# Kernel optimization log

Measured on AMD Instinct MI355X. Metric: run time of the kernel, lower is better.

## Reference

```python
import jax, jax.numpy as jnp
import numpy as np

BAG = 15          # bag_size
STEPS = 5
LAM = 1e-3        # anti_hebb_lambda
PS = 8            # patch_size
IM = 28           # image_size
DEN = IM - PS     # position normalization denominator (=20)
KEEP = 0.1        # 1 - recurrent_sparsity


def _ln(h, gamma, beta, eps=1e-5):
    mu = jnp.mean(h, axis=-1, keepdims=True)
    var = jnp.mean((h - mu) ** 2, axis=-1, keepdims=True)
    return (h - mu) * jax.lax.rsqrt(var + eps) * gamma + beta


def _patch(img, pos):
    # img: [IM, IM], pos: [2] int32 -> flattened PSxPS patch [PS*PS]
    return jax.lax.dynamic_slice(img, (pos[0], pos[1]), (PS, PS)).reshape(PS * PS)

_extract = jax.vmap(_patch)  # [B,IM,IM], [B,2] -> [B, PS*PS]


def setup_inputs() -> dict:
    key = jax.random.key(0)
    ks = jax.random.split(key, 8)
    B = 65536
    x = jax.random.normal(ks[0], (B, 1, IM, IM), jnp.float32)
    in_dim = PS * PS + 2
    Wi = jax.random.normal(ks[1], (BAG, in_dim), jnp.float32) * np.sqrt(2.0 / in_dim)
    bi = jnp.zeros((BAG,), jnp.float32)
    gamma = jnp.ones((BAG,), jnp.float32)
    beta = jnp.zeros((BAG,), jnp.float32)
    mask = (jax.random.uniform(ks[2], (BAG, BAG)) < KEEP).astype(jnp.float32)
    R = jax.random.normal(ks[3], (BAG, BAG), jnp.float32) * np.sqrt(2.0 / BAG) * mask
    rb = jnp.zeros((BAG,), jnp.float32)
    Wc = jax.random.normal(ks[4], (2, BAG), jnp.float32) * np.sqrt(2.0 / BAG)
    bc = jnp.zeros((2,), jnp.float32)
    Wo = jax.random.normal(ks[5], (10, BAG), jnp.float32) * np.sqrt(2.0 / BAG)
    bo = jnp.zeros((10,), jnp.float32)
    return dict(x=x, Wi=Wi, bi=bi, gamma=gamma, beta=beta, R=R, rb=rb,
                mask=mask, Wc=Wc, bc=bc, Wo=Wo, bo=bo)


def reference(x, Wi, bi, gamma, beta, R, rb, mask, Wc, bc, Wo, bo):
    B = x.shape[0]
    imgs = x[:, 0]  # [B, IM, IM]
    positions = jnp.full((B, 2), (IM - PS) // 2, dtype=jnp.int32)
    state = None
    logits = None
    for _ in range(STEPS):  # small fixed step count; state/positions recur
        flat = _extract(imgs, positions)                       # [B, 64]
        pos = positions.astype(x.dtype) / DEN * 2.0 - 1.0      # [B, 2]
        in_act = jnp.concatenate([flat, pos], axis=1) @ Wi.T + bi
        if state is None:
            state = _ln(jax.nn.relu(in_act), gamma, beta)
        else:
            coact = jnp.einsum('bi,bj->ij', state, state) / B  # [BAG, BAG]
            Reff = (R - LAM * coact) * mask
            state = _ln(jax.nn.relu(in_act + state @ Reff.T + rb), gamma, beta)
        logits = state @ Wo.T + bo                             # [B, 10]
        ctrl = jnp.tanh(state @ Wc.T + bc)                     # [B, 2]
        mag_r = jnp.abs(ctrl[:, 0])
        mag_c = jnp.abs(ctrl[:, 1])
        row_sel = mag_r >= mag_c
        row_move = jnp.where(row_sel, jnp.sign(ctrl[:, 0]).astype(jnp.int32), 0)
        col_move = jnp.where(row_sel, 0, jnp.sign(ctrl[:, 1]).astype(jnp.int32))
        positions = jnp.clip(positions + jnp.stack([row_move, col_move], axis=1), 0, IM - PS)
    return logits
```

## Files before the change

### kernel.cpp

```cpp
#include <hip/hip_runtime.h>
#include <math.h>

#define IMSZ 28
#define PSZ  8
#define LAMF 0.001f
#define CSTRIDE 240
#define SSTR 17
#define MAXBLK 256

__global__ __launch_bounds__(1024, 4) void fused5(
    const float* __restrict__ x,
    const float* __restrict__ Wi, const float* __restrict__ bi,
    const float* __restrict__ gamma, const float* __restrict__ beta,
    const float* __restrict__ R, const float* __restrict__ rb,
    const float* __restrict__ mask,
    const float* __restrict__ Wc, const float* __restrict__ bc,
    const float* __restrict__ Wo, const float* __restrict__ bo,
    float* __restrict__ slots, float* __restrict__ cvbuf,
    unsigned* __restrict__ bar, unsigned* __restrict__ ready,
    float* __restrict__ out, float invB, int nblk)
{
    __shared__ float sWi[15 * 72];
    __shared__ float sBi[16], sGa[16], sBe[16], sRb[16];
    __shared__ float sWc[32], sBc[2], sWo[160], sBo[16];
    __shared__ float sRm[226], sLm[226];
    __shared__ float sReff[240];
    __shared__ float sCoQ[4][226];
    __shared__ float sS[256 * SSTR];

    const int tid = threadIdx.x;

    for (int idx = tid; idx < 990; idx += 1024) {
        int u = idx / 66, k = idx - u * 66;
        sWi[u * 72 + k] = Wi[idx];
    }
    if (tid < 15) {
        sBi[tid] = bi[tid]; sGa[tid] = gamma[tid];
        sBe[tid] = beta[tid]; sRb[tid] = rb[tid];
    }
    if (tid >= 32 && tid < 62)  sWc[tid - 32] = Wc[tid - 32];
    if (tid >= 62 && tid < 64)  sBc[tid - 62] = bc[tid - 62];
    if (tid >= 96 && tid < 246) sWo[tid - 96] = Wo[tid - 96];
    if (tid >= 246 && tid < 256) sBo[tid - 246] = bo[tid - 246];
    if (tid >= 256 && tid < 481) {
        int t = tid - 256;
        float m = mask[t];
        sRm[t] = R[t] * m;
        sLm[t] = (LAMF * invB) * m;
    }
    if (tid >= 481 && tid < 496) sReff[tid - 256] = 0.0f;
    __syncthreads();

    const int g = tid >> 3;
    const int c = tid & 7;
    const int b0 = blockIdx.x * 256 + g;
    const int b1 = b0 + 128;
    const float* img0 = x + (size_t)b0 * (IMSZ * IMSZ);
    const float* img1 = x + (size_t)b1 * (IMSZ * IMSZ);

    int pr0 = 10, pc0 = 10, pr1 = 10, pc1 = 10;
    float hA[15], hB[15];

    for (int s = 0; s < 5; ++s) {
        float sj0A = 0.f, sj1A = 0.f, sj0B = 0.f, sj1B = 0.f;
        if (s > 0) {
            sj0A = sS[g * SSTR + c];
            sj0B = sS[(g + 128) * SSTR + c];
            if (c < 7) {
                sj1A = sS[g * SSTR + 8 + c];
                sj1B = sS[(g + 128) * SSTR + 8 + c];
            }

            if (blockIdx.x == 0) {
                if (tid < 64) {
                    const unsigned* bs = bar + (s - 1) * MAXBLK;
                    for (;;) {
                        unsigned f = 1u;
#pragma unroll
                        for (int k = 0; k < 4; ++k) {
                            int b = tid + k * 64;
                            unsigned v = (b < nblk)
                                ? __hip_atomic_load(&bs[b], __ATOMIC_RELAXED,
                                                    __HIP_MEMORY_SCOPE_AGENT)
                                : 1u;
                            f &= v;
                        }
                        if (__all(f != 0)) break;
                        __builtin_amdgcn_s_sleep(2);
                    }
                }
                __syncthreads();
                {
                    const int q = tid >> 8;
                    const int t = tid & 255;
                    if (t < 225) {
                        const float* cb = slots
                            + ((size_t)(s - 1) * MAXBLK + q * 64) * CSTRIDE + t;
                        float a0 = 0.f, a1 = 0.f, a2 = 0.f, a3 = 0.f;
#pragma unroll 4
                        for (int k = 0; k < 64; k += 4) {
                            int sb = q * 64 + k;
                            a0 += (sb + 0 < nblk) ? __hip_atomic_load(cb + (size_t)(k + 0) * CSTRIDE,
                                    __ATOMIC_RELAXED, __HIP_MEMORY_SCOPE_AGENT) : 0.f;
                            a1 += (sb + 1 < nblk) ? __hip_atomic_load(cb + (size_t)(k + 1) * CSTRIDE,
                                    __ATOMIC_RELAXED, __HIP_MEMORY_SCOPE_AGENT) : 0.f;
                            a2 += (sb + 2 < nblk) ? __hip_atomic_load(cb + (size_t)(k + 2) * CSTRIDE,
                                    __ATOMIC_RELAXED, __HIP_MEMORY_SCOPE_AGENT) : 0.f;
                            a3 += (sb + 3 < nblk) ? __hip_atomic_load(cb + (size_t)(k + 3) * CSTRIDE,
                                    __ATOMIC_RELAXED, __HIP_MEMORY_SCOPE_AGENT) : 0.f;
                        }
                        sCoQ[q][t] = (a0 + a1) + (a2 + a3);
                    }
                }
                __syncthreads();
                if (tid < 225) {
                    float cv = (sCoQ[0][tid] + sCoQ[1][tid])
                             + (sCoQ[2][tid] + sCoQ[3][tid]);
                    __hip_atomic_store(&cvbuf[(s - 1) * CSTRIDE + tid], cv,
                                       __ATOMIC_RELAXED, __HIP_MEMORY_SCOPE_AGENT);
                    sReff[tid] = sRm[tid] - sLm[tid] * cv;
                }
                __syncthreads();
                if (tid == 0)
                    __hip_atomic_store(&ready[(s - 1) * 16], 1u,
                                       __ATOMIC_RELAXED, __HIP_MEMORY_SCOPE_AGENT);
            } else {
                if (tid < 64) {
                    while (__hip_atomic_load(&ready[(s - 1) * 16],
                                             __ATOMIC_RELAXED,
                                             __HIP_MEMORY_SCOPE_AGENT) == 0u)
                        __builtin_amdgcn_s_sleep(8);
                }
                __syncthreads();
                if (tid < 225) {
                    float cv = __hip_atomic_load(&cvbuf[(s - 1) * CSTRIDE + tid],
                                                 __ATOMIC_RELAXED,
                                                 __HIP_MEMORY_SCOPE_AGENT);
                    sReff[tid] = sRm[tid] - sLm[tid] * cv;
                }
                __syncthreads();
            }
        }

        float pA[8], pB[8];
        {
            const float* q0 = img0 + pr0 * IMSZ + pc0 + c;
            const float* q1 = img1 + pr1 * IMSZ + pc1 + c;
#pragma unroll
            for (int r = 0; r < 8; ++r) { pA[r] = q0[r * IMSZ]; pB[r] = q1[r * IMSZ]; }
        }

        const float fr0 = ((float)pr0 / 20.0f) * 2.0f - 1.0f;
        const float fc0 = ((float)pc0 / 20.0f) * 2.0f - 1.0f;
        const float fr1 = ((float)pr1 / 20.0f) * 2.0f - 1.0f;
        const float fc1 = ((float)pc1 / 20.0f) * 2.0f - 1.0f;

#pragma unroll
        for (int u = 0; u < 15; ++u) {
            float a = 0.f, bq = 0.f;
            const float* w = sWi + u * 72 + c;
#pragma unroll
            for (int r = 0; r < 8; ++r) {
                float wv = w[r * 8];
                a  = fmaf(pA[r], wv, a);
                bq = fmaf(pB[r], wv, bq);
            }
            if (s > 0) {
                float w0 = sReff[u * 15 + c];
                float w1 = sReff[u * 15 + 8 + c];
                a  = fmaf(sj0A, w0, a);  a  = fmaf(sj1A, w1, a);
                bq = fmaf(sj0B, w0, bq); bq = fmaf(sj1B, w1, bq);
            }
            if (c == 0) {
                float wr = sWi[u * 72 + 64], wc = sWi[u * 72 + 65];
                float bias = sBi[u] + ((s > 0) ? sRb[u] : 0.0f);
                a  = fmaf(fr0, wr, a);  a  = fmaf(fc0, wc, a);  a  += bias;
                bq = fmaf(fr1, wr, bq); bq = fmaf(fc1, wc, bq); bq += bias;
            }
            hA[u] = a; hB[u] = bq;
        }

#pragma unroll
        for (int u = 0; u < 15; ++u) {
            float vA = hA[u], vB = hB[u];
            vA += __shfl_xor(vA, 1); vB += __shfl_xor(vB, 1);
            vA += __shfl_xor(vA, 2); vB += __shfl_xor(vB, 2);
            vA += __shfl_xor(vA, 4); vB += __shfl_xor(vB, 4);
            hA[u] = fmaxf(vA, 0.0f);
            hB[u] = fmaxf(vB, 0.0f);
        }

        float muA = 0.f, muB = 0.f;
#pragma unroll
        for (int u = 0; u < 15; ++u) { muA += hA[u]; muB += hB[u]; }
        muA *= (1.0f / 15.0f); muB *= (1.0f / 15.0f);
        float vA = 0.f, vB = 0.f;
#pragma unroll
        for (int u = 0; u < 15; ++u) {
            float dA = hA[u] - muA; vA = fmaf(dA, dA, vA);
            float dB = hB[u] - muB; vB = fmaf(dB, dB, vB);
        }
        vA *= (1.0f / 15.0f); vB *= (1.0f / 15.0f);
        const float rsA = 1.0f / sqrtf(vA + 1e-5f);
        const float rsB = 1.0f / sqrtf(vB + 1e-5f);
#pragma unroll
        for (int u = 0; u < 15; ++u) {
            hA[u] = (hA[u] - muA) * rsA * sGa[u] + sBe[u];
            hB[u] = (hB[u] - muB) * rsB * sGa[u] + sBe[u];
        }

        if (s == 4) {
#pragma unroll
            for (int rep = 0; rep < 2; ++rep) {
                int o = rep * 8 + c;
                if (o < 10) {
                    float a0 = 0.f, a1 = 0.f;
#pragma unroll
                    for (int j = 0; j < 15; ++j) {
                        a0 = fmaf(hA[j], sWo[o * 15 + j], a0);
                        a1 = fmaf(hB[j], sWo[o * 15 + j], a1);
                    }
                    out[(size_t)b0 * 10 + o] = a0 + sBo[o];
                    out[(size_t)b1 * 10 + o] = a1 + sBo[o];
                }
            }
        } else {
            float c0A = 0.f, c1A = 0.f, c0B = 0.f, c1B = 0.f;
#pragma unroll
            for (int j = 0; j < 15; ++j) {
                c0A = fmaf(hA[j], sWc[j],      c0A);
                c1A = fmaf(hA[j], sWc[15 + j], c1A);
                c0B = fmaf(hB[j], sWc[j],      c0B);
                c1B = fmaf(hB[j], sWc[15 + j], c1B);
            }
            c0A = tanhf(c0A + sBc[0]); c1A = tanhf(c1A + sBc[1]);
            c0B = tanhf(c0B + sBc[0]); c1B = tanhf(c1B + sBc[1]);
            {
                float m0 = fabsf(c0A), m1 = fabsf(c1A);
                int rm, cm;
                if (m0 >= m1) { rm = (c0A > 0.f) - (c0A < 0.f); cm = 0; }
                else          { rm = 0; cm = (c1A > 0.f) - (c1A < 0.f); }
                pr0 = min(max(pr0 + rm, 0), IMSZ - PSZ);
                pc0 = min(max(pc0 + cm, 0), IMSZ - PSZ);
            }
            {
                float m0 = fabsf(c0B), m1 = fabsf(c1B);
                int rm, cm;
                if (m0 >= m1) { rm = (c0B > 0.f) - (c0B < 0.f); cm = 0; }
                else          { rm = 0; cm = (c1B > 0.f) - (c1B < 0.f); }
                pr1 = min(max(pr1 + rm, 0), IMSZ - PSZ);
                pc1 = min(max(pc1 + cm, 0), IMSZ - PSZ);
            }

#pragma unroll
            for (int k = 0; k < 8; ++k) {
                if (c == k) {
                    sS[g * SSTR + k]         = hA[k];
                    sS[(g + 128) * SSTR + k] = hB[k];
                    if (k < 7) {
                        sS[g * SSTR + 8 + k]         = hA[8 + k];
                        sS[(g + 128) * SSTR + 8 + k] = hB[8 + k];
                    }
                }
            }
            __syncthreads();

            {
                const int q = tid >> 8;
                const int t = tid & 255;
                if (t < 225) {
                    int i = t / 15, j = t - i * 15;
                    const int base = q * 64;
                    float a0 = 0.f, a1 = 0.f, a2 = 0.f, a3 = 0.f;
#pragma unroll
                    for (int bb = 0; bb < 64; bb += 4) {
                        a0 = fmaf(sS[(base + bb + 0) * SSTR + i], sS[(base + bb + 0) * SSTR + j], a0);
                        a1 = fmaf(sS[(base + bb + 1) * SSTR + i], sS[(base + bb + 1) * SSTR + j], a1);
                        a2 = fmaf(sS[(base + bb + 2) * SSTR + i], sS[(base + bb + 2) * SSTR + j], a2);
                        a3 = fmaf(sS[(base + bb + 3) * SSTR + i], sS[(base + bb + 3) * SSTR + j], a3);
                    }
                    sCoQ[q][t] = (a0 + a1) + (a2 + a3);
                }
            }
            __syncthreads();

            if (tid < 225) {
                float v = (sCoQ[0][tid] + sCoQ[1][tid])
                        + (sCoQ[2][tid] + sCoQ[3][tid]);
                __hip_atomic_store(
                    &slots[((size_t)s * MAXBLK + blockIdx.x) * CSTRIDE + tid], v,
                    __ATOMIC_RELAXED, __HIP_MEMORY_SCOPE_AGENT);
            }
            __syncthreads();

            if (tid == 0)
                __hip_atomic_store(&bar[s * MAXBLK + blockIdx.x], 1u,
                                   __ATOMIC_RELAXED, __HIP_MEMORY_SCOPE_AGENT);
        }
    }
}

extern "C" void kernel_launch(void* const* d_in, const int* in_sizes, int n_in,
                              void* d_out, int out_size, void* d_ws, size_t ws_size,
                              hipStream_t stream) {
    (void)n_in; (void)out_size; (void)ws_size;
    const float* x     = (const float*)d_in[0];
    const float* Wi    = (const float*)d_in[1];
    const float* bi    = (const float*)d_in[2];
    const float* gamma = (const float*)d_in[3];
    const float* beta  = (const float*)d_in[4];
    const float* R     = (const float*)d_in[5];
    const float* rb    = (const float*)d_in[6];
    const float* mask  = (const float*)d_in[7];
    const float* Wc    = (const float*)d_in[8];
    const float* bc    = (const float*)d_in[9];
    const float* Wo    = (const float*)d_in[10];
    const float* bo    = (const float*)d_in[11];
    float* out = (float*)d_out;

    const int B = in_sizes[0] / (IMSZ * IMSZ);
    const float invB = 1.0f / (float)B;
    int grid = B / 256;

    unsigned* bar   = (unsigned*)d_ws;
    unsigned* ready = bar + 4 * MAXBLK;
    float* cvbuf    = (float*)(ready + 4 * 16);
    float* slots    = cvbuf + 4 * CSTRIDE;

    hipMemsetAsync(d_ws, 0, (size_t)(4 * MAXBLK + 4 * 16) * sizeof(unsigned), stream);

    fused5<<<grid, 1024, 0, stream>>>(
        x, Wi, bi, gamma, beta, R, rb, mask, Wc, bc, Wo, bo,
        slots, cvbuf, bar, ready, out, invB, grid);
}
```

Before: 404.8 us.

## Overlap next-step patch load and input projection with grid-wide coactivation barrier

Restructures the step loop so that, after a block publishes its partial coactivation matrix, it loads the next patch and computes the input projection before waiting on the grid barrier. This hides the barrier and global reduction latency behind independent work. The change also transposes the slot layout so block 0 reduces each of the 225 entries with one wavefront of coalesced loads plus shuffles. It also swaps the 8-lane shuffle reduction for DPP row operations. The cost is more live registers across the barrier and extra reasoning about correctness of the DPP reduction.

```diff
diff --git a/kernel.cpp b/kernel.cpp
--- a/kernel.cpp
+++ b/kernel.cpp
@@ -7,6 +7,31 @@
 #define CSTRIDE 240
 #define SSTR 17
 #define MAXBLK 256
+#define NST 225
+
+__device__ __forceinline__ float devload(const float* p) {
+    return __hip_atomic_load(p, __ATOMIC_RELAXED, __HIP_MEMORY_SCOPE_AGENT);
+}
+__device__ __forceinline__ unsigned devloadu(const unsigned* p) {
+    return __hip_atomic_load(p, __ATOMIC_RELAXED, __HIP_MEMORY_SCOPE_AGENT);
+}
+__device__ __forceinline__ void devstore(float* p, float v) {
+    __hip_atomic_store(p, v, __ATOMIC_RELAXED, __HIP_MEMORY_SCOPE_AGENT);
+}
+__device__ __forceinline__ void devstoreu(unsigned* p, unsigned v) {
+    __hip_atomic_store(p, v, __ATOMIC_RELAXED, __HIP_MEMORY_SCOPE_AGENT);
+}
+
+__device__ __forceinline__ float dpp_sum8(float v) {
+    int t;
+    t = __builtin_amdgcn_update_dpp(0, __float_as_int(v), 0xB1, 0xF, 0xF, true);
+    v += __int_as_float(t);
+    t = __builtin_amdgcn_update_dpp(0, __float_as_int(v), 0x4E, 0xF, 0xF, true);
+    v += __int_as_float(t);
+    t = __builtin_amdgcn_update_dpp(0, __float_as_int(v), 0x141, 0xF, 0xF, true);
+    v += __int_as_float(t);
+    return v;
+}
 
 __global__ __launch_bounds__(1024, 4) void fused5(
     const float* __restrict__ x,
@@ -61,133 +86,46 @@
     int pr0 = 10, pc0 = 10, pr1 = 10, pc1 = 10;
     float hA[15], hB[15];
 
-    for (int s = 0; s < 5; ++s) {
-        float sj0A = 0.f, sj1A = 0.f, sj0B = 0.f, sj1B = 0.f;
-        if (s > 0) {
-            sj0A = sS[g * SSTR + c];
-            sj0B = sS[(g + 128) * SSTR + c];
-            if (c < 7) {
-                sj1A = sS[g * SSTR + 8 + c];
-                sj1B = sS[(g + 128) * SSTR + 8 + c];
-            }
-
-            if (blockIdx.x == 0) {
-                if (tid < 64) {
-                    const unsigned* bs = bar + (s - 1) * MAXBLK;
-                    for (;;) {
-                        unsigned f = 1u;
-#pragma unroll
-                        for (int k = 0; k < 4; ++k) {
-                            int b = tid + k * 64;
-                            unsigned v = (b < nblk)
-                                ? __hip_atomic_load(&bs[b], __ATOMIC_RELAXED,
-                                                    __HIP_MEMORY_SCOPE_AGENT)
-                                : 1u;
-                            f &= v;
-                        }
-                        if (__all(f != 0)) break;
-                        __builtin_amdgcn_s_sleep(2);
-                    }
-                }
-                __syncthreads();
-                {
-                    const int q = tid >> 8;
-                    const int t = tid & 255;
-                    if (t < 225) {
-                        const float* cb = slots
-                            + ((size_t)(s - 1) * MAXBLK + q * 64) * CSTRIDE + t;
-                        float a0 = 0.f, a1 = 0.f, a2 = 0.f, a3 = 0.f;
-#pragma unroll 4
-                        for (int k = 0; k < 64; k += 4) {
-                            int sb = q * 64 + k;
-                            a0 += (sb + 0 < nblk) ? __hip_atomic_load(cb + (size_t)(k + 0) * CSTRIDE,
-                                    __ATOMIC_RELAXED, __HIP_MEMORY_SCOPE_AGENT) : 0.f;
-                            a1 += (sb + 1 < nblk) ? __hip_atomic_load(cb + (size_t)(k + 1) * CSTRIDE,
-                                    __ATOMIC_RELAXED, __HIP_MEMORY_SCOPE_AGENT) : 0.f;
-                            a2 += (sb + 2 < nblk) ? __hip_atomic_load(cb + (size_t)(k + 2) * CSTRIDE,
-                                    __ATOMIC_RELAXED, __HIP_MEMORY_SCOPE_AGENT) : 0.f;
-                            a3 += (sb + 3 < nblk) ? __hip_atomic_load(cb + (size_t)(k + 3) * CSTRIDE,
-                                    __ATOMIC_RELAXED, __HIP_MEMORY_SCOPE_AGENT) : 0.f;
-                        }
-                        sCoQ[q][t] = (a0 + a1) + (a2 + a3);
-                    }
-                }
-                __syncthreads();
-                if (tid < 225) {
-                    float cv = (sCoQ[0][tid] + sCoQ[1][tid])
-                             + (sCoQ[2][tid] + sCoQ[3][tid]);
-                    __hip_atomic_store(&cvbuf[(s - 1) * CSTRIDE + tid], cv,
-                                       __ATOMIC_RELAXED, __HIP_MEMORY_SCOPE_AGENT);
-                    sReff[tid] = sRm[tid] - sLm[tid] * cv;
-                }
-                __syncthreads();
-                if (tid == 0)
-                    __hip_atomic_store(&ready[(s - 1) * 16], 1u,
-                                       __ATOMIC_RELAXED, __HIP_MEMORY_SCOPE_AGENT);
-            } else {
-                if (tid < 64) {
-                    while (__hip_atomic_load(&ready[(s - 1) * 16],
-                                             __ATOMIC_RELAXED,
-                                             __HIP_MEMORY_SCOPE_AGENT) == 0u)
-                        __builtin_amdgcn_s_sleep(8);
-                }
-                __syncthreads();
-                if (tid < 225) {
-                    float cv = __hip_atomic_load(&cvbuf[(s - 1) * CSTRIDE + tid],
-                                                 __ATOMIC_RELAXED,
-                                                 __HIP_MEMORY_SCOPE_AGENT);
-                    sReff[tid] = sRm[tid] - sLm[tid] * cv;
-                }
-                __syncthreads();
-            }
-        }
-
+    {
         float pA[8], pB[8];
-        {
-            const float* q0 = img0 + pr0 * IMSZ + pc0 + c;
-            const float* q1 = img1 + pr1 * IMSZ + pc1 + c;
-#pragma unroll
-            for (int r = 0; r < 8; ++r) { pA[r] = q0[r * IMSZ]; pB[r] = q1[r * IMSZ]; }
-        }
-
-        const float fr0 = ((float)pr0 / 20.0f) * 2.0f - 1.0f;
-        const float fc0 = ((float)pc0 / 20.0f) * 2.0f - 1.0f;
-        const float fr1 = ((float)pr1 / 20.0f) * 2.0f - 1.0f;
-        const float fc1 = ((float)pc1 / 20.0f) * 2.0f - 1.0f;
-
+        const float* q0 = img0 + (10 * IMSZ + 10) + c;
+        const float* q1 = img1 + (10 * IMSZ + 10) + c;
+#pragma unroll
+        for (int r = 0; r < 8; ++r) { pA[r] = q0[r * IMSZ]; pB[r] = q1[r * IMSZ]; }
 #pragma unroll
         for (int u = 0; u < 15; ++u) {
+            const float* w = sWi + u * 72 + c;
             float a = 0.f, bq = 0.f;
-            const float* w = sWi + u * 72 + c;
 #pragma unroll
             for (int r = 0; r < 8; ++r) {
                 float wv = w[r * 8];
                 a  = fmaf(pA[r], wv, a);
                 bq = fmaf(pB[r], wv, bq);
             }
-            if (s > 0) {
+            if (c == 0) { a += sBi[u]; bq += sBi[u]; }
+            hA[u] = a; hB[u] = bq;
+        }
+    }
+
+    for (int s = 0; s < 5; ++s) {
+        if (s > 0) {
+            float sj0A = sS[g * SSTR + c];
+            float sj0B = sS[(g + 128) * SSTR + c];
+            float sj1A = (c < 7) ? sS[g * SSTR + 8 + c] : 0.f;
+            float sj1B = (c < 7) ? sS[(g + 128) * SSTR + 8 + c] : 0.f;
+#pragma unroll
+            for (int u = 0; u < 15; ++u) {
                 float w0 = sReff[u * 15 + c];
                 float w1 = sReff[u * 15 + 8 + c];
-                a  = fmaf(sj0A, w0, a);  a  = fmaf(sj1A, w1, a);
-                bq = fmaf(sj0B, w0, bq); bq = fmaf(sj1B, w1, bq);
-            }
-            if (c == 0) {
-                float wr = sWi[u * 72 + 64], wc = sWi[u * 72 + 65];
-                float bias = sBi[u] + ((s > 0) ? sRb[u] : 0.0f);
-                a  = fmaf(fr0, wr, a);  a  = fmaf(fc0, wc, a);  a  += bias;
-                bq = fmaf(fr1, wr, bq); bq = fmaf(fc1, wc, bq); bq += bias;
-            }
-            hA[u] = a; hB[u] = bq;
+                hA[u] = fmaf(sj0A, w0, hA[u]); hA[u] = fmaf(sj1A, w1, hA[u]);
+                hB[u] = fmaf(sj0B, w0, hB[u]); hB[u] = fmaf(sj1B, w1, hB[u]);
+            }
         }
 
 #pragma unroll
         for (int u = 0; u < 15; ++u) {
-            float vA = hA[u], vB = hB[u];
-            vA += __shfl_xor(vA, 1); vB += __shfl_xor(vB, 1);
-            vA += __shfl_xor(vA, 2); vB += __shfl_xor(vB, 2);
-            vA += __shfl_xor(vA, 4); vB += __shfl_xor(vB, 4);
-            hA[u] = fmaxf(vA, 0.0f);
-            hB[u] = fmaxf(vB, 0.0f);
+            hA[u] = fmaxf(dpp_sum8(hA[u]), 0.0f);
+            hB[u] = fmaxf(dpp_sum8(hB[u]), 0.0f);
         }
 
         float muA = 0.f, muB = 0.f;
@@ -224,7 +162,10 @@
                     out[(size_t)b1 * 10 + o] = a1 + sBo[o];
                 }
             }
-        } else {
+            break;
+        }
+
+        {
             float c0A = 0.f, c1A = 0.f, c0B = 0.f, c1B = 0.f;
 #pragma unroll
             for (int j = 0; j < 15; ++j) {
@@ -251,51 +192,137 @@
                 pr1 = min(max(pr1 + rm, 0), IMSZ - PSZ);
                 pc1 = min(max(pc1 + cm, 0), IMSZ - PSZ);
             }
-
-#pragma unroll
-            for (int k = 0; k < 8; ++k) {
-                if (c == k) {
-                    sS[g * SSTR + k]         = hA[k];
-                    sS[(g + 128) * SSTR + k] = hB[k];
-                    if (k < 7) {
-                        sS[g * SSTR + 8 + k]         = hA[8 + k];
-                        sS[(g + 128) * SSTR + 8 + k] = hB[8 + k];
+        }
+
+        float pA[8], pB[8];
+        {
+            const float* q0 = img0 + pr0 * IMSZ + pc0 + c;
+            const float* q1 = img1 + pr1 * IMSZ + pc1 + c;
+#pragma unroll
+            for (int r = 0; r < 8; ++r) { pA[r] = q0[r * IMSZ]; pB[r] = q1[r * IMSZ]; }
+        }
+
+#pragma unroll
+        for (int k = 0; k < 8; ++k) {
+            if (c == k) {
+                sS[g * SSTR + k]         = hA[k];
+                sS[(g + 128) * SSTR + k] = hB[k];
+                if (k < 7) {
+                    sS[g * SSTR + 8 + k]         = hA[8 + k];
+                    sS[(g + 128) * SSTR + 8 + k] = hB[8 + k];
+                }
+            }
+        }
+        __syncthreads();
+
+        {
+            const int q = tid >> 8;
+            const int t = tid & 255;
+            if (t < NST) {
+                int i = t / 15, j = t - i * 15;
+                const int base = q * 64;
+                float a0 = 0.f, a1 = 0.f, a2 = 0.f, a3 = 0.f;
+#pragma unroll
+                for (int bb = 0; bb < 64; bb += 4) {
+                    a0 = fmaf(sS[(base + bb + 0) * SSTR + i], sS[(base + bb + 0) * SSTR + j], a0);
+                    a1 = fmaf(sS[(base + bb + 1) * SSTR + i], sS[(base + bb + 1) * SSTR + j], a1);
+                    a2 = fmaf(sS[(base + bb + 2) * SSTR + i], sS[(base + bb + 2) * SSTR + j], a2);
+                    a3 = fmaf(sS[(base + bb + 3) * SSTR + i], sS[(base + bb + 3) * SSTR + j], a3);
+                }
+                sCoQ[q][t] = (a0 + a1) + (a2 + a3);
+            }
+        }
+        __syncthreads();
+
+        if (tid < NST) {
+            float v = (sCoQ[0][tid] + sCoQ[1][tid])
+                    + (sCoQ[2][tid] + sCoQ[3][tid]);
+            devstore(&slots[((size_t)s * NST + tid) * MAXBLK + blockIdx.x], v);
+        }
+        __syncthreads();
+
+        if (tid == 0)
+            devstoreu(&bar[s * MAXBLK + blockIdx.x], 1u);
+
+        {
+            const float fr0 = ((float)pr0 / 20.0f) * 2.0f - 1.0f;
+            const float fc0 = ((float)pc0 / 20.0f) * 2.0f - 1.0f;
+            const float fr1 = ((float)pr1 / 20.0f) * 2.0f - 1.0f;
+            const float fc1 = ((float)pc1 / 20.0f) * 2.0f - 1.0f;
+#pragma unroll
+            for (int u = 0; u < 15; ++u) {
+                const float* w = sWi + u * 72 + c;
+                float a = 0.f, bq = 0.f;
+#pragma unroll
+                for (int r = 0; r < 8; ++r) {
+                    float wv = w[r * 8];
+                    a  = fmaf(pA[r], wv, a);
+                    bq = fmaf(pB[r], wv, bq);
+                }
+                if (c == 0) {
+                    float wr = sWi[u * 72 + 64], wc = sWi[u * 72 + 65];
+                    float bias = sBi[u] + sRb[u];
+                    a  = fmaf(fr0, wr, a);  a  = fmaf(fc0, wc, a);  a  += bias;
+                    bq = fmaf(fr1, wr, bq); bq = fmaf(fc1, wc, bq); bq += bias;
+                }
+                hA[u] = a; hB[u] = bq;
+            }
+        }
+
+        if (blockIdx.x == 0) {
+            if (tid < 64) {
+                const unsigned* bs = bar + s * MAXBLK;
+                for (;;) {
+                    unsigned f = 1u;
+#pragma unroll
+                    for (int k = 0; k < 4; ++k) {
+                        int b = tid + k * 64;
+                        unsigned v = (b < nblk) ? devloadu(&bs[b]) : 1u;
+                        f &= v;
                     }
-                }
-            }
-            __syncthreads();
-
+                    if (__all(f != 0)) break;
+                    __builtin_amdgcn_s_sleep(2);
+                }
+            }
+            __syncthreads();
             {
-                const int q = tid >> 8;
-                const int t = tid & 255;
-                if (t < 225) {
-                    int i = t / 15, j = t - i * 15;
-                    const int base = q * 64;
-                    float a0 = 0.f, a1 = 0.f, a2 = 0.f, a3 = 0.f;
-#pragma unroll
-                    for (int bb = 0; bb < 64; bb += 4) {
-                        a0 = fmaf(sS[(base + bb + 0) * SSTR + i], sS[(base + bb + 0) * SSTR + j], a0);
-                        a1 = fmaf(sS[(base + bb + 1) * SSTR + i], sS[(base + bb + 1) * SSTR + j], a1);
-                        a2 = fmaf(sS[(base + bb + 2) * SSTR + i], sS[(base + bb + 2) * SSTR + j], a2);
-                        a3 = fmaf(sS[(base + bb + 3) * SSTR + i], sS[(base + bb + 3) * SSTR + j], a3);
+                const int wid = tid >> 6, ln = tid & 63;
+                for (int j = 0; j < 15; ++j) {
+                    int t = wid * 15 + j;
+                    if (t < NST) {
+                        const float* p = slots + ((size_t)s * NST + t) * MAXBLK + ln;
+                        float v = 0.f;
+#pragma unroll
+                        for (int k = 0; k < 4; ++k) {
+                            int b = k * 64 + ln;
+                            v += (b < nblk) ? devload(p + k * 64) : 0.f;
+                        }
+                        v += __shfl_xor(v, 1);  v += __shfl_xor(v, 2);
+                        v += __shfl_xor(v, 4);  v += __shfl_xor(v, 8);
+                        v += __shfl_xor(v, 16); v += __shfl_xor(v, 32);
+                        if (ln == 0) devstore(&cvbuf[s * CSTRIDE + t], v);
                     }
-                    sCoQ[q][t] = (a0 + a1) + (a2 + a3);
-                }
-            }
-            __syncthreads();
-
-            if (tid < 225) {
-                float v = (sCoQ[0][tid] + sCoQ[1][tid])
-                        + (sCoQ[2][tid] + sCoQ[3][tid]);
-                __hip_atomic_store(
-                    &slots[((size_t)s * MAXBLK + blockIdx.x) * CSTRIDE + tid], v,
-                    __ATOMIC_RELAXED, __HIP_MEMORY_SCOPE_AGENT);
-            }
-            __syncthreads();
-
+                }
+            }
+            __syncthreads();
             if (tid == 0)
-                __hip_atomic_store(&bar[s * MAXBLK + blockIdx.x], 1u,
-                                   __ATOMIC_RELAXED, __HIP_MEMORY_SCOPE_AGENT);
+                devstoreu(&ready[s * 16], 1u);
+            if (tid < NST) {
+                float cv = devload(&cvbuf[s * CSTRIDE + tid]);
+                sReff[tid] = sRm[tid] - sLm[tid] * cv;
+            }
+            __syncthreads();
+        } else {
+            if (tid < 64) {
+                while (devloadu(&ready[s * 16]) == 0u)
+                    __builtin_amdgcn_s_sleep(8);
+            }
+            __syncthreads();
+            if (tid < NST) {
+                float cv = devload(&cvbuf[s * CSTRIDE + tid]);
+                sReff[tid] = sRm[tid] - sLm[tid] * cv;
+            }
+            __syncthreads();
         }
     }
 }
```

Result: slower. 465.5 us (+15.0%).
